# Performance work log

Measured on AMD Instinct MI355X. Metric: run time of the kernel, lower is better.

Reference implementation:

```python
import jax, jax.numpy as jnp
import numpy as np
import math

D_MODEL = 1024
HIDDEN = 1024
NUM_HEADS = 16
D_K = D_MODEL // NUM_HEADS  # 64
B, S = 4, 2048


def setup_inputs() -> dict:
    key = jax.random.key(0)
    ks = jax.random.split(key, 11)
    sc_in = 1.0 / math.sqrt(D_MODEL)
    sc_h = 1.0 / math.sqrt(HIDDEN)
    return {
        "k": jax.random.normal(ks[0], (B, S, D_MODEL), jnp.float32),
        "q": jax.random.normal(ks[1], (B, S, D_MODEL), jnp.float32),
        "v": jax.random.normal(ks[2], (B, S, D_MODEL), jnp.float32),
        "Wq": jax.random.normal(ks[3], (HIDDEN, D_MODEL), jnp.float32) * sc_in,
        "bq": jnp.zeros((HIDDEN,), jnp.float32),
        "Wk": jax.random.normal(ks[4], (HIDDEN, D_MODEL), jnp.float32) * sc_in,
        "bk": jnp.zeros((HIDDEN,), jnp.float32),
        "Wv": jax.random.normal(ks[5], (HIDDEN, D_MODEL), jnp.float32) * sc_in,
        "bv": jnp.zeros((HIDDEN,), jnp.float32),
        "Wo": jax.random.normal(ks[6], (HIDDEN, HIDDEN), jnp.float32) * sc_h,
        "bo": jnp.zeros((HIDDEN,), jnp.float32),
    }


def _split_heads(x):
    # [B, S, HIDDEN] -> [B, H, S, d_k]
    b, s, _ = x.shape
    return x.reshape(b, s, NUM_HEADS, D_K).transpose(0, 2, 1, 3)


def reference(k, q, v, Wq, bq, Wk, bk, Wv, bv, Wo, bo):
    qp = _split_heads(q @ Wq.T + bq)
    kp = _split_heads(k @ Wk.T + bk)
    vp = _split_heads(v @ Wv.T + bv)
    inv_sqrt_dk = 1.0 / math.sqrt(D_K)
    # [B, H, Sq, Sk]
    mult = jnp.einsum("bhqd,bhkd->bhqk", qp, kp) * inv_sqrt_dk
    # torch f.softmax without dim on a 4D tensor -> dim=1 (heads axis)
    w = jax.nn.softmax(mult, axis=1)
    w = jax.nn.softmax(w * inv_sqrt_dk, axis=1)  # second softmax, same implicit dim
    val = jnp.einsum("bhqk,bhkd->bhqd", w, vp)
    val = val.transpose(0, 2, 1, 3).reshape(q.shape[0], q.shape[1], HIDDEN)
    return val @ Wo.T + bo
```

## Files before the change

### kernel.cpp

```cpp
#include <hip/hip_runtime.h>
#include <math.h>

#define BB 4
#define SS 2048
#define DM 1024
#define NH 16

typedef unsigned short u16;
typedef __attribute__((ext_vector_type(8))) short bf16x8;
typedef __attribute__((ext_vector_type(4))) float f32x4;

__device__ __forceinline__ u16 f2bf(float f) {
  union { float f; unsigned u; } v; v.f = f;
  unsigned r = v.u + 0x7fffu + ((v.u >> 16) & 1u);
  return (u16)(r >> 16);
}
__device__ __forceinline__ float bf2f(u16 h) {
  union { unsigned u; float f; } v; v.u = ((unsigned)h) << 16;
  return v.f;
}
__device__ __forceinline__ void gl16(const u16* g, u16* l) {
  __builtin_amdgcn_global_load_lds((__attribute__((address_space(1))) void*)(u16*)g,
                                   (__attribute__((address_space(3))) void*)l, 16, 0, 0);
}

__global__ __launch_bounds__(256) void cvt_bf16(const float* __restrict__ in,
                                                u16* __restrict__ out, int n8) {
  int i = blockIdx.x * 256 + threadIdx.x;
  if (i >= n8) return;
  const float4* p = (const float4*)in + (size_t)i * 2;
  float4 a = p[0], b = p[1];
  ushort4 o0 = { f2bf(a.x), f2bf(a.y), f2bf(a.z), f2bf(a.w) };
  ushort4 o1 = { f2bf(b.x), f2bf(b.y), f2bf(b.z), f2bf(b.w) };
  ushort4* q = (ushort4*)out + (size_t)i * 2;
  q[0] = o0; q[1] = o1;
}

template <int MODE>
__global__ __launch_bounds__(256) void gemm_proj(const u16* __restrict__ A,
                                                 const u16* __restrict__ W,
                                                 const float* __restrict__ bias,
                                                 void* __restrict__ Cv,
                                                 int M, int N, int K) {
  __shared__ __align__(16) u16 As[128 * 32];
  __shared__ __align__(16) u16 Bs[128 * 32];
  const int t = threadIdx.x;
  const int w = t >> 6, l = t & 63;
  const int m0 = blockIdx.x * 128, n0 = blockIdx.y * 128;
  const int wm = (w >> 1) * 64, wn = (w & 1) * 64;
  const int lr = l & 15, lg = (l >> 4) * 8;
  const int sr = t >> 2, sc4 = (t & 3) * 8;

  const u16* Ap1 = A + (size_t)(m0 + sr) * K + sc4;
  const u16* Ap2 = Ap1 + (size_t)64 * K;
  const u16* Wp1 = W + (size_t)(n0 + sr) * K + sc4;
  const u16* Wp2 = Wp1 + (size_t)64 * K;
  u16* Asd1 = As + w * 512;
  u16* Asd2 = As + 2048 + w * 512;
  u16* Bsd1 = Bs + w * 512;
  u16* Bsd2 = Bs + 2048 + w * 512;

  f32x4 acc[4][4];
  f32x4 z4 = {0.f, 0.f, 0.f, 0.f};
#pragma unroll
  for (int i = 0; i < 4; ++i)
#pragma unroll
    for (int j = 0; j < 4; ++j) acc[i][j] = z4;

  for (int k0 = 0; k0 < K; k0 += 32) {
    __syncthreads();
    gl16(Ap1 + k0, Asd1);
    gl16(Ap2 + k0, Asd2);
    gl16(Wp1 + k0, Bsd1);
    gl16(Wp2 + k0, Bsd2);
    __syncthreads();
    bf16x8 af[4], bw[4];
#pragma unroll
    for (int i = 0; i < 4; ++i) {
      af[i] = *(const bf16x8*)&As[(wm + i * 16 + lr) * 32 + lg];
      bw[i] = *(const bf16x8*)&Bs[(wn + i * 16 + lr) * 32 + lg];
    }
#pragma unroll
    for (int i = 0; i < 4; ++i)
#pragma unroll
      for (int j = 0; j < 4; ++j)
        acc[i][j] = __builtin_amdgcn_mfma_f32_16x16x32_bf16(af[i], bw[j], acc[i][j], 0, 0, 0);
  }

  const int lg4 = (l >> 4) * 4;
#pragma unroll
  for (int j = 0; j < 4; ++j) {
    const int col = n0 + wn + j * 16 + lr;
    const float bj = bias[col];
#pragma unroll
    for (int i = 0; i < 4; ++i) {
#pragma unroll
      for (int r = 0; r < 4; ++r) {
        const int row = m0 + wm + i * 16 + lg4 + r;
        const float val = acc[i][j][r] + bj;
        if (MODE == 0) {
          ((u16*)Cv)[(size_t)row * N + col] = f2bf(val);
        } else if (MODE == 1) {
          ((u16*)Cv)[((size_t)((row >> 11) * 16 + (col >> 6)) * 64 + (col & 63)) * SS +
                     (row & 2047)] = f2bf(val);
        } else {
          ((float*)Cv)[(size_t)row * N + col] = val;
        }
      }
    }
  }
}

__device__ __forceinline__ void dsm16(float x[16]) {
  float m = x[0];
#pragma unroll
  for (int h = 1; h < 16; ++h) m = fmaxf(m, x[h]);
  float s = 0.f;
#pragma unroll
  for (int h = 0; h < 16; ++h) { x[h] = __expf(x[h] - m); s += x[h]; }
  const float inv = 0.125f / s;
  float s2 = 0.f;
#pragma unroll
  for (int h = 0; h < 16; ++h) { x[h] = __expf((x[h] - 1.0f) * inv); s2 += x[h]; }
  const float inv2 = 1.f / s2;
#pragma unroll
  for (int h = 0; h < 16; ++h) x[h] *= inv2;
}

__global__ __launch_bounds__(512, 2) void fused_attn(const u16* __restrict__ Qp,
                                                     const u16* __restrict__ Kp,
                                                     const u16* __restrict__ Vt,
                                                     u16* __restrict__ AO) {
  __shared__ __align__(16) u16 Ks[32 * 1024];
  __shared__ __align__(16) u16 Vs[1024 * 32];
  __shared__ __align__(16) u16 Ws[16 * 32 * 32];

  const int t = threadIdx.x;
  const int w = t >> 6, l = t & 63;
  const int lr = l & 15, lg = l >> 4;
  const int bid = blockIdx.x;
  const int xcd = bid & 7;
  const int b = xcd >> 1;
  const int qt = (xcd & 1) * 32 + (bid >> 3);
  const int q0 = qt * 32;
  const int h0 = w * 2;

  bf16x8 qf[2][2][2];
#pragma unroll
  for (int hh = 0; hh < 2; ++hh)
#pragma unroll
    for (int m = 0; m < 2; ++m)
#pragma unroll
      for (int dc = 0; dc < 2; ++dc)
        qf[hh][m][dc] = *(const bf16x8*)(Qp + ((size_t)b * SS + q0 + m * 16 + lr) * DM +
                                         (h0 + hh) * 64 + dc * 32 + lg * 8);

  f32x4 o[2][2][4];
  f32x4 z4 = {0.f, 0.f, 0.f, 0.f};
#pragma unroll
  for (int hh = 0; hh < 2; ++hh)
#pragma unroll
    for (int m = 0; m < 2; ++m)
#pragma unroll
      for (int d = 0; d < 4; ++d) o[hh][m][d] = z4;

  const int sq = t >> 4;
  const int sk = t & 15;

  for (int k0 = 0; k0 < SS; k0 += 32) {
#pragma unroll
    for (int call = 0; call < 8; ++call) {
      const int p = call * 512 + t;
      const int r = p >> 7, c = p & 127;
      const int cg = (c & ~7) | ((c ^ r) & 7);
      gl16(Kp + ((size_t)b * SS + k0 + r) * DM + cg * 8, Ks + p * 8);
    }
#pragma unroll
    for (int call = 0; call < 8; ++call) {
      const int p = call * 512 + t;
      const int d = p >> 2, c = p & 3;
      gl16(Vt + ((size_t)b * 1024 + d) * SS + k0 + c * 8, Vs + p * 8);
    }
    __syncthreads();

    f32x4 sa[2][2][2];
#pragma unroll
    for (int hh = 0; hh < 2; ++hh)
#pragma unroll
      for (int n = 0; n < 2; ++n)
#pragma unroll
        for (int m = 0; m < 2; ++m) sa[hh][n][m] = z4;
#pragma unroll
    for (int hh = 0; hh < 2; ++hh)
#pragma unroll
      for (int dc = 0; dc < 2; ++dc)
#pragma unroll
        for (int n = 0; n < 2; ++n) {
          const int row = n * 16 + lr;
          const int cl = (dc * 4 + lg) ^ (row & 7);
          bf16x8 kf = *(const bf16x8*)&Ks[row * 1024 + (h0 + hh) * 64 + cl * 8];
#pragma unroll
          for (int m = 0; m < 2; ++m)
            sa[hh][n][m] =
                __builtin_amdgcn_mfma_f32_16x16x32_bf16(kf, qf[hh][m][dc], sa[hh][n][m], 0, 0, 0);
        }
#pragma unroll
    for (int hh = 0; hh < 2; ++hh)
#pragma unroll
      for (int n = 0; n < 2; ++n)
#pragma unroll
        for (int m = 0; m < 2; ++m) {
          ushort4 pk = { f2bf(sa[hh][n][m][0] * 0.125f), f2bf(sa[hh][n][m][1] * 0.125f),
                         f2bf(sa[hh][n][m][2] * 0.125f), f2bf(sa[hh][n][m][3] * 0.125f) };
          *(ushort4*)&Ws[(h0 + hh) * 1024 + (m * 16 + lr) * 32 + n * 16 + lg * 4] = pk;
        }
    __syncthreads();

    {
      u16* fib = Ws + sq * 32 + sk * 2;
      float xa[16], xb[16];
#pragma unroll
      for (int h = 0; h < 16; ++h) {
        const unsigned u = *(const unsigned*)(fib + h * 1024);
        xa[h] = bf2f((u16)(u & 0xffffu));
        xb[h] = bf2f((u16)(u >> 16));
      }
      dsm16(xa);
      dsm16(xb);
#pragma unroll
      for (int h = 0; h < 16; ++h)
        *(unsigned*)(fib + h * 1024) = (unsigned)f2bf(xa[h]) | ((unsigned)f2bf(xb[h]) << 16);
    }
    __syncthreads();

#pragma unroll
    for (int hh = 0; hh < 2; ++hh) {
      bf16x8 aw[2];
#pragma unroll
      for (int m = 0; m < 2; ++m)
        aw[m] = *(const bf16x8*)&Ws[(h0 + hh) * 1024 + (m * 16 + lr) * 32 + lg * 8];
#pragma unroll
      for (int ds = 0; ds < 4; ++ds) {
        bf16x8 vf = *(const bf16x8*)&Vs[((h0 + hh) * 64 + ds * 16 + lr) * 32 + lg * 8];
#pragma unroll
        for (int m = 0; m < 2; ++m)
          o[hh][m][ds] =
              __builtin_amdgcn_mfma_f32_16x16x32_bf16(aw[m], vf, o[hh][m][ds], 0, 0, 0);
      }
    }
    __syncthreads();
  }

#pragma unroll
  for (int hh = 0; hh < 2; ++hh)
#pragma unroll
    for (int m = 0; m < 2; ++m)
#pragma unroll
      for (int ds = 0; ds < 4; ++ds)
#pragma unroll
        for (int r = 0; r < 4; ++r)
          AO[((size_t)b * SS + q0 + m * 16 + lg * 4 + r) * DM + (h0 + hh) * 64 + ds * 16 + lr] =
              f2bf(o[hh][m][ds][r]);
}

extern "C" void kernel_launch(void* const* d_in, const int* in_sizes, int n_in,
                              void* d_out, int out_size, void* d_ws, size_t ws_size,
                              hipStream_t stream) {
  const float* kin = (const float*)d_in[0];
  const float* qin = (const float*)d_in[1];
  const float* vin = (const float*)d_in[2];
  const float* Wq  = (const float*)d_in[3];
  const float* bq  = (const float*)d_in[4];
  const float* Wk  = (const float*)d_in[5];
  const float* bk  = (const float*)d_in[6];
  const float* Wv  = (const float*)d_in[7];
  const float* bv  = (const float*)d_in[8];
  const float* Wo  = (const float*)d_in[9];
  const float* bo  = (const float*)d_in[10];

  const size_t P   = (size_t)BB * SS * DM;
  const size_t WSZ = (size_t)DM * DM;
  u16* Qb  = (u16*)d_ws;
  u16* Kb  = Qb + P;
  u16* Vb  = Kb + P;
  u16* Wqb = Vb + P;
  u16* Wkb = Wqb + WSZ;
  u16* Wvb = Wkb + WSZ;
  u16* Wob = Wvb + WSZ;
  u16* Qp  = Wob + WSZ;
  u16* Kp  = Qp + P;
  u16* Vt  = Kp + P;
  u16* AO  = Vt + P;

  cvt_bf16<<<dim3(4096), 256, 0, stream>>>(qin, Qb, (int)(P / 8));
  cvt_bf16<<<dim3(4096), 256, 0, stream>>>(kin, Kb, (int)(P / 8));
  cvt_bf16<<<dim3(4096), 256, 0, stream>>>(vin, Vb, (int)(P / 8));
  cvt_bf16<<<dim3(512), 256, 0, stream>>>(Wq, Wqb, (int)(WSZ / 8));
  cvt_bf16<<<dim3(512), 256, 0, stream>>>(Wk, Wkb, (int)(WSZ / 8));
  cvt_bf16<<<dim3(512), 256, 0, stream>>>(Wv, Wvb, (int)(WSZ / 8));
  cvt_bf16<<<dim3(512), 256, 0, stream>>>(Wo, Wob, (int)(WSZ / 8));

  dim3 gp(64, 8);
  gemm_proj<0><<<gp, 256, 0, stream>>>(Qb, Wqb, bq, Qp, 8192, 1024, 1024);
  gemm_proj<0><<<gp, 256, 0, stream>>>(Kb, Wkb, bk, Kp, 8192, 1024, 1024);
  gemm_proj<1><<<gp, 256, 0, stream>>>(Vb, Wvb, bv, Vt, 8192, 1024, 1024);

  fused_attn<<<dim3(256), 512, 0, stream>>>(Qp, Kp, Vt, AO);

  gemm_proj<2><<<gp, 256, 0, stream>>>(AO, Wob, bo, (float*)d_out, 8192, 1024, 1024);
}
```

Before: 702.2 us.

## Double-buffer K tiles in LDS and load V fragments directly into registers

K tiles are now double-buffered in shared memory, and the next tile's async global-to-LDS load is issued during the softmax phase so it overlaps compute. V is no longer staged through LDS; each wave loads its own V fragments straight from global memory into registers at the top of each iteration, with precomputed pointers. This removes one LDS staging buffer and hides K load latency. In exchange the V global loads become per-wave and uncoalesced-ish, and register pressure rises under a 512x2 launch bound. The last iteration also prefetches one tile past the end of K.

```diff
diff --git a/kernel.cpp b/kernel.cpp
--- a/kernel.cpp
+++ b/kernel.cpp
@@ -131,8 +131,7 @@
                                                      const u16* __restrict__ Kp,
                                                      const u16* __restrict__ Vt,
                                                      u16* __restrict__ AO) {
-  __shared__ __align__(16) u16 Ks[32 * 1024];
-  __shared__ __align__(16) u16 Vs[1024 * 32];
+  __shared__ __align__(16) u16 Ks[2][32 * 1024];
   __shared__ __align__(16) u16 Ws[16 * 32 * 32];
 
   const int t = threadIdx.x;
@@ -155,6 +154,22 @@
         qf[hh][m][dc] = *(const bf16x8*)(Qp + ((size_t)b * SS + q0 + m * 16 + lr) * DM +
                                          (h0 + hh) * 64 + dc * 32 + lg * 8);
 
+  const u16* kaddr[8];
+#pragma unroll
+  for (int i = 0; i < 8; ++i) {
+    const int p = i * 512 + t;
+    const int r = p >> 7, c = p & 127;
+    const int cg = (c & ~7) | ((c ^ r) & 7);
+    kaddr[i] = Kp + ((size_t)b * SS + r) * DM + cg * 8;
+  }
+  const u16* vp[8];
+#pragma unroll
+  for (int hh = 0; hh < 2; ++hh)
+#pragma unroll
+    for (int ds = 0; ds < 4; ++ds)
+      vp[hh * 4 + ds] =
+          Vt + (((size_t)b * 16 + h0 + hh) * 64 + ds * 16 + lr) * SS + lg * 8;
+
   f32x4 o[2][2][4];
   f32x4 z4 = {0.f, 0.f, 0.f, 0.f};
 #pragma unroll
@@ -167,21 +182,24 @@
   const int sq = t >> 4;
   const int sk = t & 15;
 
-  for (int k0 = 0; k0 < SS; k0 += 32) {
-#pragma unroll
-    for (int call = 0; call < 8; ++call) {
-      const int p = call * 512 + t;
-      const int r = p >> 7, c = p & 127;
-      const int cg = (c & ~7) | ((c ^ r) & 7);
-      gl16(Kp + ((size_t)b * SS + k0 + r) * DM + cg * 8, Ks + p * 8);
-    }
-#pragma unroll
-    for (int call = 0; call < 8; ++call) {
-      const int p = call * 512 + t;
-      const int d = p >> 2, c = p & 3;
-      gl16(Vt + ((size_t)b * 1024 + d) * SS + k0 + c * 8, Vs + p * 8);
-    }
-    __syncthreads();
+#pragma unroll
+  for (int i = 0; i < 8; ++i) {
+    gl16(kaddr[i], &Ks[0][0] + (i * 512 + t) * 8);
+    kaddr[i] += 32;
+  }
+  __syncthreads();
+
+  for (int tti = 0; tti < 64; ++tti) {
+    const int cur = tti & 1;
+    u16* KsC = &Ks[cur][0];
+    u16* KsN = &Ks[cur ^ 1][0];
+
+    bf16x8 vfr[8];
+#pragma unroll
+    for (int i = 0; i < 8; ++i) {
+      vfr[i] = *(const bf16x8*)vp[i];
+      vp[i] += 32;
+    }
 
     f32x4 sa[2][2][2];
 #pragma unroll
@@ -198,7 +216,7 @@
         for (int n = 0; n < 2; ++n) {
           const int row = n * 16 + lr;
           const int cl = (dc * 4 + lg) ^ (row & 7);
-          bf16x8 kf = *(const bf16x8*)&Ks[row * 1024 + (h0 + hh) * 64 + cl * 8];
+          bf16x8 kf = *(const bf16x8*)&KsC[row * 1024 + (h0 + hh) * 64 + cl * 8];
 #pragma unroll
           for (int m = 0; m < 2; ++m)
             sa[hh][n][m] =
@@ -216,6 +234,11 @@
         }
     __syncthreads();
 
+#pragma unroll
+    for (int i = 0; i < 8; ++i) {
+      gl16(kaddr[i], KsN + (i * 512 + t) * 8);
+      kaddr[i] += 32;
+    }
     {
       u16* fib = Ws + sq * 32 + sk * 2;
       float xa[16], xb[16];
@@ -241,11 +264,10 @@
         aw[m] = *(const bf16x8*)&Ws[(h0 + hh) * 1024 + (m * 16 + lr) * 32 + lg * 8];
 #pragma unroll
       for (int ds = 0; ds < 4; ++ds) {
-        bf16x8 vf = *(const bf16x8*)&Vs[((h0 + hh) * 64 + ds * 16 + lr) * 32 + lg * 8];
 #pragma unroll
         for (int m = 0; m < 2; ++m)
-          o[hh][m][ds] =
-              __builtin_amdgcn_mfma_f32_16x16x32_bf16(aw[m], vf, o[hh][m][ds], 0, 0, 0);
+          o[hh][m][ds] = __builtin_amdgcn_mfma_f32_16x16x32_bf16(aw[m], vfr[hh * 4 + ds],
+                                                                 o[hh][m][ds], 0, 0, 0);
       }
     }
     __syncthreads();
```

After: 578.3 us. -17.6%, faster.

## Load K/V fragments directly into registers with prefetch, double-buffer score LDS

Applied to the files above, without the earlier changes.

Drops the shared-memory staging of K and V tiles. Each wave now loads its own K and V MFMA fragments straight from global memory into registers, prefetching the next tile while the current one is processed. The score buffer is double-buffered and padded to a 40-element row stride, which removes the end-of-iteration barrier and the LDS bank conflicts. The price is more vector registers and uncoalesced 16-byte global loads that depend on L2 hits, since the LDS-based sharing across waves is gone.

```diff
diff --git a/kernel.cpp b/kernel.cpp
--- a/kernel.cpp
+++ b/kernel.cpp
@@ -23,6 +23,14 @@
   __builtin_amdgcn_global_load_lds((__attribute__((address_space(1))) void*)(u16*)g,
                                    (__attribute__((address_space(3))) void*)l, 16, 0, 0);
 }
+
+#define BARRIER_LDS()                                    \
+  do {                                                   \
+    __builtin_amdgcn_sched_barrier(0);                   \
+    asm volatile("s_waitcnt lgkmcnt(0)" ::: "memory");   \
+    __builtin_amdgcn_s_barrier();                        \
+    __builtin_amdgcn_sched_barrier(0);                   \
+  } while (0)
 
 __global__ __launch_bounds__(256) void cvt_bf16(const float* __restrict__ in,
                                                 u16* __restrict__ out, int n8) {
@@ -127,13 +135,13 @@
   for (int h = 0; h < 16; ++h) x[h] *= inv2;
 }
 
+#define WROW 40
+#define WPLANE (32 * WROW)
 __global__ __launch_bounds__(512, 2) void fused_attn(const u16* __restrict__ Qp,
                                                      const u16* __restrict__ Kp,
                                                      const u16* __restrict__ Vt,
                                                      u16* __restrict__ AO) {
-  __shared__ __align__(16) u16 Ks[32 * 1024];
-  __shared__ __align__(16) u16 Vs[1024 * 32];
-  __shared__ __align__(16) u16 Ws[16 * 32 * 32];
+  __shared__ __align__(16) u16 Ws[2][16 * WPLANE];
 
   const int t = threadIdx.x;
   const int w = t >> 6, l = t & 63;
@@ -155,6 +163,9 @@
         qf[hh][m][dc] = *(const bf16x8*)(Qp + ((size_t)b * SS + q0 + m * 16 + lr) * DM +
                                          (h0 + hh) * 64 + dc * 32 + lg * 8);
 
+  const u16* kb = Kp + ((size_t)b * SS + lr) * DM + h0 * 64 + lg * 8;
+  const u16* vb = Vt + (((size_t)b * 16 + h0) * 64 + lr) * SS + lg * 8;
+
   f32x4 o[2][2][4];
   f32x4 z4 = {0.f, 0.f, 0.f, 0.f};
 #pragma unroll
@@ -167,21 +178,25 @@
   const int sq = t >> 4;
   const int sk = t & 15;
 
-  for (int k0 = 0; k0 < SS; k0 += 32) {
-#pragma unroll
-    for (int call = 0; call < 8; ++call) {
-      const int p = call * 512 + t;
-      const int r = p >> 7, c = p & 127;
-      const int cg = (c & ~7) | ((c ^ r) & 7);
-      gl16(Kp + ((size_t)b * SS + k0 + r) * DM + cg * 8, Ks + p * 8);
-    }
-#pragma unroll
-    for (int call = 0; call < 8; ++call) {
-      const int p = call * 512 + t;
-      const int d = p >> 2, c = p & 3;
-      gl16(Vt + ((size_t)b * 1024 + d) * SS + k0 + c * 8, Vs + p * 8);
-    }
-    __syncthreads();
+  bf16x8 kfr[8], vfr[8];
+#pragma unroll
+  for (int hh = 0; hh < 2; ++hh)
+#pragma unroll
+    for (int dc = 0; dc < 2; ++dc)
+#pragma unroll
+      for (int n = 0; n < 2; ++n)
+        kfr[hh * 4 + dc * 2 + n] =
+            *(const bf16x8*)(kb + (size_t)(n * 16) * DM + hh * 64 + dc * 32);
+#pragma unroll
+  for (int hh = 0; hh < 2; ++hh)
+#pragma unroll
+    for (int ds = 0; ds < 4; ++ds)
+      vfr[hh * 4 + ds] = *(const bf16x8*)(vb + (size_t)(hh * 64 + ds * 16) * SS);
+
+  for (int tt = 0; tt < 64; ++tt) {
+    u16* Wsb = &Ws[tt & 1][0];
+    const size_t knext = (size_t)(((tt + 1) & 63) * 32) * DM;
+    const int vnext = ((tt + 1) & 63) * 32;
 
     f32x4 sa[2][2][2];
 #pragma unroll
@@ -195,15 +210,11 @@
 #pragma unroll
       for (int dc = 0; dc < 2; ++dc)
 #pragma unroll
-        for (int n = 0; n < 2; ++n) {
-          const int row = n * 16 + lr;
-          const int cl = (dc * 4 + lg) ^ (row & 7);
-          bf16x8 kf = *(const bf16x8*)&Ks[row * 1024 + (h0 + hh) * 64 + cl * 8];
+        for (int n = 0; n < 2; ++n)
 #pragma unroll
           for (int m = 0; m < 2; ++m)
-            sa[hh][n][m] =
-                __builtin_amdgcn_mfma_f32_16x16x32_bf16(kf, qf[hh][m][dc], sa[hh][n][m], 0, 0, 0);
-        }
+            sa[hh][n][m] = __builtin_amdgcn_mfma_f32_16x16x32_bf16(
+                kfr[hh * 4 + dc * 2 + n], qf[hh][m][dc], sa[hh][n][m], 0, 0, 0);
 #pragma unroll
     for (int hh = 0; hh < 2; ++hh)
 #pragma unroll
@@ -212,16 +223,24 @@
         for (int m = 0; m < 2; ++m) {
           ushort4 pk = { f2bf(sa[hh][n][m][0] * 0.125f), f2bf(sa[hh][n][m][1] * 0.125f),
                          f2bf(sa[hh][n][m][2] * 0.125f), f2bf(sa[hh][n][m][3] * 0.125f) };
-          *(ushort4*)&Ws[(h0 + hh) * 1024 + (m * 16 + lr) * 32 + n * 16 + lg * 4] = pk;
+          *(ushort4*)&Wsb[(h0 + hh) * WPLANE + (m * 16 + lr) * WROW + n * 16 + lg * 4] = pk;
         }
-    __syncthreads();
+#pragma unroll
+    for (int hh = 0; hh < 2; ++hh)
+#pragma unroll
+      for (int dc = 0; dc < 2; ++dc)
+#pragma unroll
+        for (int n = 0; n < 2; ++n)
+          kfr[hh * 4 + dc * 2 + n] =
+              *(const bf16x8*)(kb + knext + (size_t)(n * 16) * DM + hh * 64 + dc * 32);
+    BARRIER_LDS();
 
     {
-      u16* fib = Ws + sq * 32 + sk * 2;
+      u16* fib = Wsb + sq * WROW + sk * 2;
       float xa[16], xb[16];
 #pragma unroll
       for (int h = 0; h < 16; ++h) {
-        const unsigned u = *(const unsigned*)(fib + h * 1024);
+        const unsigned u = *(const unsigned*)(fib + h * WPLANE);
         xa[h] = bf2f((u16)(u & 0xffffu));
         xb[h] = bf2f((u16)(u >> 16));
       }
@@ -229,26 +248,28 @@
       dsm16(xb);
 #pragma unroll
       for (int h = 0; h < 16; ++h)
-        *(unsigned*)(fib + h * 1024) = (unsigned)f2bf(xa[h]) | ((unsigned)f2bf(xb[h]) << 16);
+        *(unsigned*)(fib + h * WPLANE) = (unsigned)f2bf(xa[h]) | ((unsigned)f2bf(xb[h]) << 16);
     }
-    __syncthreads();
+    BARRIER_LDS();
 
 #pragma unroll
     for (int hh = 0; hh < 2; ++hh) {
       bf16x8 aw[2];
 #pragma unroll
       for (int m = 0; m < 2; ++m)
-        aw[m] = *(const bf16x8*)&Ws[(h0 + hh) * 1024 + (m * 16 + lr) * 32 + lg * 8];
-#pragma unroll
-      for (int ds = 0; ds < 4; ++ds) {
-        bf16x8 vf = *(const bf16x8*)&Vs[((h0 + hh) * 64 + ds * 16 + lr) * 32 + lg * 8];
+        aw[m] = *(const bf16x8*)&Wsb[(h0 + hh) * WPLANE + (m * 16 + lr) * WROW + lg * 8];
+#pragma unroll
+      for (int ds = 0; ds < 4; ++ds)
 #pragma unroll
         for (int m = 0; m < 2; ++m)
-          o[hh][m][ds] =
-              __builtin_amdgcn_mfma_f32_16x16x32_bf16(aw[m], vf, o[hh][m][ds], 0, 0, 0);
-      }
+          o[hh][m][ds] = __builtin_amdgcn_mfma_f32_16x16x32_bf16(aw[m], vfr[hh * 4 + ds],
+                                                                 o[hh][m][ds], 0, 0, 0);
     }
-    __syncthreads();
+#pragma unroll
+    for (int hh = 0; hh < 2; ++hh)
+#pragma unroll
+      for (int ds = 0; ds < 4; ++ds)
+        vfr[hh * 4 + ds] = *(const bf16x8*)(vb + vnext + (size_t)(hh * 64 + ds * 16) * SS);
   }
 
 #pragma unroll
```

Result: faster. 627.0 us (-10.7%).
